# Kernel optimization log

Hardware: AMD Instinct MI355X
Metric: run time of the kernel (lower is better)

Reference implementation:

```python
import jax, jax.numpy as jnp
import numpy as np

K = 4
TEMPERATURE = 34.0
IN_CH = 256
OUT_CH = 256
KSIZE = 3
PAD = 1
HIDDEN = int(2 * IN_CH * 0.25) + 1  # pool_mode='mix' doubles channels -> 129


def setup_inputs() -> dict:
    key = jax.random.key(0)
    ks = jax.random.split(key, 6)
    x = jax.random.normal(ks[0], (32, IN_CH, 56, 56), dtype=jnp.float32)
    # dynamic kernel bank [K, O, C, k, k]
    weight = jax.random.normal(ks[1], (K, OUT_CH, IN_CH, KSIZE, KSIZE), dtype=jnp.float32) * 0.05
    bias_k = jnp.zeros((K, OUT_CH), dtype=jnp.float32)
    # attention MLP (1x1 convs on pooled [B, 2C, 1, 1] == linear layers)
    w1 = jax.random.normal(ks[2], (HIDDEN, 2 * IN_CH), dtype=jnp.float32) * 0.06  # fc1, no bias
    w2 = jax.random.normal(ks[3], (K, HIDDEN), dtype=jnp.float32) * 0.12
    b2 = jnp.zeros((K,), dtype=jnp.float32)
    return {"x": x, "weight": weight, "bias_k": bias_k, "w1": w1, "w2": w2, "b2": b2}


def _attention(x, w1, w2, b2):
    # mix pooling: concat(avg, max) over spatial dims -> [B, 2C]
    avg = jnp.mean(x, axis=(2, 3))
    mx = jnp.max(x, axis=(2, 3))
    p = jnp.concatenate([avg, mx], axis=1)
    h = jax.nn.relu(jnp.einsum('bc,hc->bh', p, w1))
    logits = jnp.einsum('bh,kh->bk', h, w2) + b2
    return jax.nn.softmax(logits / TEMPERATURE, axis=1)  # [B, K]


def reference(x, weight, bias_k, w1, w2, b2):
    B, C, H, W = x.shape
    attn = _attention(x, w1, w2, b2)  # [B, K]
    # per-sample aggregated kernels [B, O, C, k, k]
    agg_w = jnp.einsum('bk,kocuv->bocuv', attn, weight)
    agg_b = attn @ bias_k  # [B, O]
    # grouped-conv trick: treat batch as groups
    xg = x.reshape(1, B * C, H, W)
    wg = agg_w.reshape(B * OUT_CH, C, KSIZE, KSIZE)
    out = jax.lax.conv_general_dilated(
        xg, wg,
        window_strides=(1, 1),
        padding=[(PAD, PAD), (PAD, PAD)],
        dimension_numbers=('NCHW', 'OIHW', 'NCHW'),
        feature_group_count=B,
    )  # [1, B*O, H, W]
    out = out.reshape(B, OUT_CH, H, W) + agg_b[:, :, None, None]
    return out
```

## Files before the change

kernel.cpp:

```cpp
#include <hip/hip_runtime.h>
#include <math.h>

#define BB 32
#define CC 256
#define OO 256
#define HW 56
#define SP (HW*HW)
#define KK 4
#define HID 129
#define TEMP 34.0f
#define CPAD 40

typedef unsigned short u16;
typedef unsigned int uint32;
typedef __attribute__((ext_vector_type(8))) short bf16x8;
typedef __attribute__((ext_vector_type(4))) float f32x4;

__device__ __forceinline__ u16 f2bf(float f) {
    union { float f; uint32 u; } v; v.f = f;
    uint32 r = v.u + 0x7FFF + ((v.u >> 16) & 1);
    return (u16)(r >> 16);
}

__global__ __launch_bounds__(256) void trans_pool(const float* __restrict__ x,
                                                  u16* __restrict__ xt,
                                                  float* __restrict__ pooled) {
    const int cb = blockIdx.x, b = blockIdx.y;
    const int tid = threadIdx.x;
    const int lane = tid & 63, wave = tid >> 6;
    const float* xp = x + ((size_t)b * CC + cb * 32) * SP;
    u16* xtb = xt + (size_t)(b * 8 + cb) * SP * 32;

    float psum[32], pmax[32];
    #pragma unroll
    for (int c = 0; c < 32; ++c) { psum[c] = 0.f; pmax[c] = -INFINITY; }

    for (int p0 = 0; p0 < SP; p0 += 256) {
        const int p = p0 + tid;
        const bool v = p < SP;
        const int pc = v ? p : (SP - 1);
        u16 ob[32];
        #pragma unroll
        for (int c = 0; c < 32; ++c) {
            const float vv = xp[(size_t)c * SP + pc];
            if (v) { psum[c] += vv; pmax[c] = fmaxf(pmax[c], vv); }
            ob[c] = f2bf(vv);
        }
        if (v) {
            #pragma unroll
            for (int j = 0; j < 4; ++j)
                *(bf16x8*)&xtb[(size_t)p * 32 + j * 8] = *(bf16x8*)&ob[j * 8];
        }
    }
    #pragma unroll
    for (int c = 0; c < 32; ++c) {
        #pragma unroll
        for (int off = 32; off >= 1; off >>= 1) {
            psum[c] += __shfl_xor(psum[c], off, 64);
            pmax[c] = fmaxf(pmax[c], __shfl_xor(pmax[c], off, 64));
        }
    }
    __shared__ float ssum[4][32];
    __shared__ float smax[4][32];
    if (lane == 0) {
        #pragma unroll
        for (int c = 0; c < 32; ++c) { ssum[wave][c] = psum[c]; smax[wave][c] = pmax[c]; }
    }
    __syncthreads();
    if (tid < 32) {
        const float s = ssum[0][tid] + ssum[1][tid] + ssum[2][tid] + ssum[3][tid];
        const float m = fmaxf(fmaxf(smax[0][tid], smax[1][tid]),
                              fmaxf(smax[2][tid], smax[3][tid]));
        pooled[b * (2 * CC) + cb * 32 + tid]      = s / (float)SP;
        pooled[b * (2 * CC) + CC + cb * 32 + tid] = m;
    }
}

__global__ __launch_bounds__(256) void attn_kernel(const float* __restrict__ pooled,
                                                   const float* __restrict__ w1,
                                                   const float* __restrict__ w2,
                                                   const float* __restrict__ b2,
                                                   const float* __restrict__ bias_k,
                                                   float* __restrict__ attn,
                                                   float* __restrict__ agg_b) {
    const int b = blockIdx.x;
    const int tid = threadIdx.x;
    __shared__ float p[2 * CC];
    __shared__ float h[HID];
    __shared__ float a[KK];
    for (int i = tid; i < 2 * CC; i += 256) p[i] = pooled[b * 2 * CC + i];
    __syncthreads();
    if (tid < HID) {
        float s = 0.f;
        const float* w1r = w1 + (size_t)tid * (2 * CC);
        for (int c = 0; c < 2 * CC; ++c) s = fmaf(p[c], w1r[c], s);
        h[tid] = fmaxf(s, 0.f);
    }
    __syncthreads();
    if (tid == 0) {
        float lg[KK];
        float m = -INFINITY;
        for (int k = 0; k < KK; ++k) {
            float s = b2[k];
            for (int i = 0; i < HID; ++i) s = fmaf(h[i], w2[k * HID + i], s);
            lg[k] = s / TEMP;
            m = fmaxf(m, lg[k]);
        }
        float den = 0.f;
        for (int k = 0; k < KK; ++k) { lg[k] = expf(lg[k] - m); den += lg[k]; }
        for (int k = 0; k < KK; ++k) { a[k] = lg[k] / den; attn[b * KK + k] = a[k]; }
    }
    __syncthreads();
    if (tid < OO) {
        float s = 0.f;
        #pragma unroll
        for (int k = 0; k < KK; ++k) s = fmaf(a[k], bias_k[k * OO + tid], s);
        agg_b[b * OO + tid] = s;
    }
}

__global__ __launch_bounds__(256) void agg_kernel(const float* __restrict__ weight,
                                                  const float* __restrict__ attn,
                                                  u16* __restrict__ wT) {
    const int o = blockIdx.x;
    const int c = threadIdx.x;
    __shared__ float at[BB * KK];
    if (threadIdx.x < BB * KK) at[threadIdx.x] = attn[threadIdx.x];
    __syncthreads();
    float w[KK][9];
    #pragma unroll
    for (int k = 0; k < KK; ++k)
        #pragma unroll
        for (int uv = 0; uv < 9; ++uv)
            w[k][uv] = weight[(size_t)((k * OO + o) * CC + c) * 9 + uv];
    for (int b = 0; b < BB; ++b) {
        const float a0 = at[b*KK+0], a1 = at[b*KK+1], a2 = at[b*KK+2], a3 = at[b*KK+3];
        #pragma unroll
        for (int uv = 0; uv < 9; ++uv) {
            float s = a0 * w[0][uv] + a1 * w[1][uv] + a2 * w[2][uv] + a3 * w[3][uv];
            wT[(size_t)((b * 9 + uv) * OO + o) * CC + c] = f2bf(s);
        }
    }
}

__global__ __launch_bounds__(256, 2) void conv_mfma(const u16* __restrict__ xt,
                                                    const u16* __restrict__ wT,
                                                    const float* __restrict__ agg_b,
                                                    float* __restrict__ out) {
    const int id   = blockIdx.x;
    const int g    = id >> 3;
    const int b    = (id & 7) + 8 * (g / 28);
    const int tile = g % 28;
    const int px   = tile % 14, oy = tile / 14;
    const int tid  = threadIdx.x;
    const int lane = tid & 63, wave = tid >> 6;
    const int wm = wave & 1, wn = wave >> 1;
    const int l15 = lane & 15, kg = lane >> 4;
    const int p0 = px * 224;
    const int r0 = px * 4 - 1;
    const int pbase = r0 * 56;
    const int b8 = b * 8;

    __shared__ u16 xs[2][6 * 58 * CPAD];

    if (tid < 96) {
        const int bufi = tid / 48, t = tid % 48;
        const int gg = t >> 2, q = t & 3;
        const int r = gg >> 1, side = gg & 1;
        bf16x8 z = {};
        *(bf16x8*)&xs[bufi][(r * 58 + side * 57) * CPAD + q * 8] = z;
    }

    int ldsoff[6]; long long goff[6]; bool vld[6], act[6];
    #pragma unroll
    for (int k = 0; k < 6; ++k) {
        const int i = tid + k * 256;
        const int s = i >> 2, q = i & 3;
        const int rrel = s / 56, col = s % 56;
        const int p = pbase + s;
        act[k] = (i < 1344);
        vld[k] = act[k] && (p >= 0) && (p < SP);
        ldsoff[k] = (rrel * 58 + col + 1) * CPAD + q * 8;
        goff[k] = (long long)p * 32 + q * 8;
    }

    int lds_base[7];
    #pragma unroll
    for (int nf = 0; nf < 7; ++nf) {
        const int n   = wn * 112 + nf * 16 + l15;
        const int rr  = n / 56 + 1;
        const int col = n % 56;
        lds_base[nf] = (rr * 58 + col + 1) * CPAD + kg * 8;
    }

    const u16* wTb = wT + (size_t)b * 9 * OO * CC
                        + (size_t)(oy * 128 + wm * 64 + l15) * CC + kg * 8;

    f32x4 acc[4][7];
    #pragma unroll
    for (int mf = 0; mf < 4; ++mf)
        #pragma unroll
        for (int nf = 0; nf < 7; ++nf)
            acc[mf][nf] = (f32x4)0.f;

    {
        bf16x8 stg[6];
        const u16* xtb = xt + (size_t)b8 * SP * 32;
        #pragma unroll
        for (int k = 0; k < 6; ++k)
            if (act[k]) stg[k] = vld[k] ? *(const bf16x8*)(xtb + goff[k]) : (bf16x8)0;
        #pragma unroll
        for (int k = 0; k < 6; ++k)
            if (act[k]) *(bf16x8*)&xs[0][ldsoff[k]] = stg[k];
    }
    __syncthreads();

    for (int cb = 0; cb < 8; ++cb) {
        bf16x8 nxt[6];
        if (cb < 7) {
            const u16* xtb = xt + (size_t)(b8 + cb + 1) * SP * 32;
            #pragma unroll
            for (int k = 0; k < 6; ++k)
                if (act[k]) nxt[k] = vld[k] ? *(const bf16x8*)(xtb + goff[k]) : (bf16x8)0;
        }

        const u16* xsb = xs[cb & 1];
        const int c0 = cb * 32;
        #pragma unroll
        for (int uv = 0; uv < 9; ++uv) {
            const int du = uv / 3 - 1, dv = uv % 3 - 1;
            const int toff = (du * 58 + dv) * CPAD;
            bf16x8 av[4];
            #pragma unroll
            for (int mf = 0; mf < 4; ++mf)
                av[mf] = *(const bf16x8*)(wTb + (size_t)uv * OO * CC + mf * 16 * CC + c0);
            #pragma unroll
            for (int nf = 0; nf < 7; ++nf) {
                const bf16x8 bv = *(const bf16x8*)&xsb[lds_base[nf] + toff];
                #pragma unroll
                for (int mf = 0; mf < 4; ++mf)
                    acc[mf][nf] = __builtin_amdgcn_mfma_f32_16x16x32_bf16(av[mf], bv, acc[mf][nf], 0, 0, 0);
            }
        }

        if (cb < 7) {
            #pragma unroll
            for (int k = 0; k < 6; ++k)
                if (act[k]) *(bf16x8*)&xs[(cb + 1) & 1][ldsoff[k]] = nxt[k];
        }
        __syncthreads();
    }

    const int obase = oy * 128 + wm * 64;
    float* outb = out + (size_t)b * OO * SP;
    #pragma unroll
    for (int mf = 0; mf < 4; ++mf) {
        #pragma unroll
        for (int r = 0; r < 4; ++r) {
            const int o = obase + mf * 16 + kg * 4 + r;
            const float bias = agg_b[b * OO + o];
            #pragma unroll
            for (int nf = 0; nf < 7; ++nf) {
                const int p = p0 + wn * 112 + nf * 16 + l15;
                outb[(size_t)o * SP + p] = acc[mf][nf][r] + bias;
            }
        }
    }
}

extern "C" void kernel_launch(void* const* d_in, const int* in_sizes, int n_in,
                              void* d_out, int out_size, void* d_ws, size_t ws_size,
                              hipStream_t stream) {
    const float* x      = (const float*)d_in[0];
    const float* weight = (const float*)d_in[1];
    const float* bias_k = (const float*)d_in[2];
    const float* w1     = (const float*)d_in[3];
    const float* w2     = (const float*)d_in[4];
    const float* b2     = (const float*)d_in[5];
    float* out = (float*)d_out;

    u16* x_t = (u16*)d_ws;
    u16* wT  = x_t + (size_t)BB * 8 * SP * 32;
    float* ws_f   = (float*)(wT + (size_t)BB * 9 * OO * CC);
    float* pooled = ws_f;
    float* attn   = ws_f + BB * 2 * CC;
    float* agg_b  = attn + BB * KK;

    trans_pool<<<dim3(8, BB), 256, 0, stream>>>(x, x_t, pooled);
    attn_kernel<<<BB, 256, 0, stream>>>(pooled, w1, w2, b2, bias_k, attn, agg_b);
    agg_kernel<<<OO, 256, 0, stream>>>(weight, attn, wT);
    conv_mfma<<<896, 256, 0, stream>>>(x_t, wT, agg_b, out);
}
```

Baseline: 228.8 us.

## Pre-pad transposed input in global memory and read conv operands directly from cache

The transpose kernel now writes x into a zero-padded 58x58 plane layout, filling the border slots itself. The conv kernel drops its LDS staging and double buffering and reads B fragments straight from global memory at shifted addresses, with no __syncthreads. This removes the LDS copy and barrier overhead. In exchange it depends on L1/L2 to serve the ninefold overlapping reuse, so B loads may now pay global latency instead of LDS latency.

```diff
diff --git a/kernel.cpp b/kernel.cpp
--- a/kernel.cpp
+++ b/kernel.cpp
@@ -9,7 +9,8 @@
 #define KK 4
 #define HID 129
 #define TEMP 34.0f
-#define CPAD 40
+#define PROW 58
+#define PLANE (PROW*PROW*32)
 
 typedef unsigned short u16;
 typedef unsigned int uint32;
@@ -29,7 +30,19 @@
     const int tid = threadIdx.x;
     const int lane = tid & 63, wave = tid >> 6;
     const float* xp = x + ((size_t)b * CC + cb * 32) * SP;
-    u16* xtb = xt + (size_t)(b * 8 + cb) * SP * 32;
+    u16* xtb = xt + (size_t)(b * 8 + cb) * PLANE;
+
+    if (tid < 228) {
+        int slot;
+        if (tid < 58)       slot = tid;
+        else if (tid < 116) slot = 57 * 58 + (tid - 58);
+        else if (tid < 172) slot = (tid - 116 + 1) * 58;
+        else                slot = (tid - 172 + 1) * 58 + 57;
+        bf16x8 z = {};
+        #pragma unroll
+        for (int j = 0; j < 4; ++j)
+            *(bf16x8*)&xtb[(size_t)slot * 32 + j * 8] = z;
+    }
 
     float psum[32], pmax[32];
     #pragma unroll
@@ -47,9 +60,10 @@
             ob[c] = f2bf(vv);
         }
         if (v) {
+            const int slot = (p / 56 + 1) * 58 + (p % 56 + 1);
             #pragma unroll
             for (int j = 0; j < 4; ++j)
-                *(bf16x8*)&xtb[(size_t)p * 32 + j * 8] = *(bf16x8*)&ob[j * 8];
+                *(bf16x8*)&xtb[(size_t)slot * 32 + j * 8] = *(bf16x8*)&ob[j * 8];
         }
     }
     #pragma unroll
@@ -157,40 +171,15 @@
     const int wm = wave & 1, wn = wave >> 1;
     const int l15 = lane & 15, kg = lane >> 4;
     const int p0 = px * 224;
-    const int r0 = px * 4 - 1;
-    const int pbase = r0 * 56;
-    const int b8 = b * 8;
-
-    __shared__ u16 xs[2][6 * 58 * CPAD];
-
-    if (tid < 96) {
-        const int bufi = tid / 48, t = tid % 48;
-        const int gg = t >> 2, q = t & 3;
-        const int r = gg >> 1, side = gg & 1;
-        bf16x8 z = {};
-        *(bf16x8*)&xs[bufi][(r * 58 + side * 57) * CPAD + q * 8] = z;
-    }
-
-    int ldsoff[6]; long long goff[6]; bool vld[6], act[6];
-    #pragma unroll
-    for (int k = 0; k < 6; ++k) {
-        const int i = tid + k * 256;
-        const int s = i >> 2, q = i & 3;
-        const int rrel = s / 56, col = s % 56;
-        const int p = pbase + s;
-        act[k] = (i < 1344);
-        vld[k] = act[k] && (p >= 0) && (p < SP);
-        ldsoff[k] = (rrel * 58 + col + 1) * CPAD + q * 8;
-        goff[k] = (long long)p * 32 + q * 8;
-    }
-
-    int lds_base[7];
+
+    const u16* xq[7];
     #pragma unroll
     for (int nf = 0; nf < 7; ++nf) {
         const int n   = wn * 112 + nf * 16 + l15;
-        const int rr  = n / 56 + 1;
+        const int R   = px * 4 + n / 56;
         const int col = n % 56;
-        lds_base[nf] = (rr * 58 + col + 1) * CPAD + kg * 8;
+        const int slot = (R + 1) * PROW + (col + 1);
+        xq[nf] = xt + (size_t)(b * 8) * PLANE + (size_t)slot * 32 + kg * 8;
     }
 
     const u16* wTb = wT + (size_t)b * 9 * OO * CC
@@ -203,52 +192,25 @@
         for (int nf = 0; nf < 7; ++nf)
             acc[mf][nf] = (f32x4)0.f;
 
-    {
-        bf16x8 stg[6];
-        const u16* xtb = xt + (size_t)b8 * SP * 32;
-        #pragma unroll
-        for (int k = 0; k < 6; ++k)
-            if (act[k]) stg[k] = vld[k] ? *(const bf16x8*)(xtb + goff[k]) : (bf16x8)0;
-        #pragma unroll
-        for (int k = 0; k < 6; ++k)
-            if (act[k]) *(bf16x8*)&xs[0][ldsoff[k]] = stg[k];
-    }
-    __syncthreads();
-
     for (int cb = 0; cb < 8; ++cb) {
-        bf16x8 nxt[6];
-        if (cb < 7) {
-            const u16* xtb = xt + (size_t)(b8 + cb + 1) * SP * 32;
-            #pragma unroll
-            for (int k = 0; k < 6; ++k)
-                if (act[k]) nxt[k] = vld[k] ? *(const bf16x8*)(xtb + goff[k]) : (bf16x8)0;
-        }
-
-        const u16* xsb = xs[cb & 1];
         const int c0 = cb * 32;
+        const size_t cplane = (size_t)cb * PLANE;
         #pragma unroll
         for (int uv = 0; uv < 9; ++uv) {
             const int du = uv / 3 - 1, dv = uv % 3 - 1;
-            const int toff = (du * 58 + dv) * CPAD;
+            const int toff = (du * PROW + dv) * 32;
             bf16x8 av[4];
             #pragma unroll
             for (int mf = 0; mf < 4; ++mf)
                 av[mf] = *(const bf16x8*)(wTb + (size_t)uv * OO * CC + mf * 16 * CC + c0);
             #pragma unroll
             for (int nf = 0; nf < 7; ++nf) {
-                const bf16x8 bv = *(const bf16x8*)&xsb[lds_base[nf] + toff];
+                const bf16x8 bv = *(const bf16x8*)(xq[nf] + cplane + toff);
                 #pragma unroll
                 for (int mf = 0; mf < 4; ++mf)
                     acc[mf][nf] = __builtin_amdgcn_mfma_f32_16x16x32_bf16(av[mf], bv, acc[mf][nf], 0, 0, 0);
             }
         }
-
-        if (cb < 7) {
-            #pragma unroll
-            for (int k = 0; k < 6; ++k)
-                if (act[k]) *(bf16x8*)&xs[(cb + 1) & 1][ldsoff[k]] = nxt[k];
-        }
-        __syncthreads();
     }
 
     const int obase = oy * 128 + wm * 64;
@@ -280,7 +242,7 @@
     float* out = (float*)d_out;
 
     u16* x_t = (u16*)d_ws;
-    u16* wT  = x_t + (size_t)BB * 8 * SP * 32;
+    u16* wT  = x_t + (size_t)BB * 8 * PLANE;
     float* ws_f   = (float*)(wT + (size_t)BB * 9 * OO * CC);
     float* pooled = ws_f;
     float* attn   = ws_f + BB * 2 * CC;
```

After: 328.6 us. 1.44x slower.
